# Kernel tuning notes

Measured on AMD Instinct MI355X. Metric: run time of the kernel, lower is better.

The kernel has to match this reference:

```python
import jax, jax.numpy as jnp
import numpy as np

EMBED = 1024
N_HEAD = 16
D_HID = EMBED // N_HEAD
R_FF = 4
D_FF = EMBED * R_FF
LN_EPS = 1e-5


def layer_norm(x, gamma, beta):
    mu = jnp.mean(x, axis=-1, keepdims=True)
    var = jnp.var(x, axis=-1, keepdims=True)
    return (x - mu) * jax.lax.rsqrt(var + LN_EPS) * gamma + beta


def setup_inputs() -> dict:
    key = jax.random.key(0)
    ks = jax.random.split(key, 10)
    B, S = 4, 2048
    # torch nn.Linear stores weight as [out, in]; y = x @ W.T
    def xavier(k, shape):
        fan_out, fan_in = shape
        lim = np.sqrt(6.0 / (fan_in + fan_out))
        return jax.random.uniform(k, shape, jnp.float32, -lim, lim)
    return {
        "x": jax.random.normal(ks[0], (B, S, EMBED), jnp.float32),
        "Wq": xavier(ks[1], (EMBED, EMBED)),
        "Wk": xavier(ks[2], (EMBED, EMBED)),
        "Wv": xavier(ks[3], (EMBED, EMBED)),
        "Wo": xavier(ks[4], (EMBED, EMBED)),
        "bo": jnp.zeros((EMBED,), jnp.float32),
        "ln1_g": jnp.ones((EMBED,), jnp.float32),
        "ln1_b": jnp.zeros((EMBED,), jnp.float32),
        "ln2_g": jnp.ones((EMBED,), jnp.float32),
        "ln2_b": jnp.zeros((EMBED,), jnp.float32),
        "W1": jax.random.normal(ks[5], (D_FF, EMBED), jnp.float32) * np.sqrt(2.0 / EMBED),
        "b1": jnp.zeros((D_FF,), jnp.float32),
        "W2": xavier(ks[6], (EMBED, D_FF)),
        "b2": jnp.zeros((EMBED,), jnp.float32),
    }


def reference(x, Wq, Wk, Wv, Wo, bo, ln1_g, ln1_b, ln2_g, ln2_b, W1, b1, W2, b2):
    B, S, E = x.shape
    scaling = 1.0 / np.sqrt(D_HID)
    # --- attention (pre-LN), dropout = identity (eval) ---
    xn = layer_norm(x, ln1_g, ln1_b)
    q = (xn @ Wq.T).reshape(B, S, N_HEAD, D_HID) * scaling
    k = (xn @ Wk.T).reshape(B, S, N_HEAD, D_HID)
    v = (xn @ Wv.T).reshape(B, S, N_HEAD, D_HID)
    scores = jnp.einsum("bqhd,bkhd->bhqk", q, k)
    attn = jax.nn.softmax(scores, axis=-1)
    out = jnp.einsum("bhqk,bkhd->bqhd", attn, v).reshape(B, S, E)
    out = out @ Wo.T + bo
    x = x + out
    # --- feed-forward (pre-LN) ---
    xn = layer_norm(x, ln2_g, ln2_b)
    h = jax.nn.relu(xn @ W1.T + b1)
    x = x + (h @ W2.T + b2)
    return x
```

## Files before the change

kernel.cpp:

```cpp
#include <hip/hip_runtime.h>
#include <hip/hip_bf16.h>
#include <cstdint>


typedef __attribute__((ext_vector_type(8))) short bf16x8;
typedef __attribute__((ext_vector_type(4))) float f32x4;

#define LDSAS __attribute__((address_space(3)))
#define GLBAS __attribute__((address_space(1)))

#define CQK 0.18033688011112044f

union APU { unsigned u[4]; bf16x8 v; };

__device__ __forceinline__ unsigned short f2bf(float f) {
  union { float f; unsigned u; } c; c.f = f;
  unsigned u = c.u + 0x7fffu + ((c.u >> 16) & 1u);
  return (unsigned short)(u >> 16);
}

__device__ __forceinline__ unsigned pk2(float a, float b) {
  __hip_bfloat162 h = __float22bfloat162_rn(make_float2(a, b));
  union { __hip_bfloat162 h; unsigned u; } c; c.h = h; return c.u;
}

__device__ __forceinline__ void async16(const unsigned short* g, unsigned short* l) {
  __builtin_amdgcn_global_load_lds((const GLBAS unsigned int*)g,
                                   (LDSAS unsigned int*)l, 16, 0, 0);
}

__global__ void cvt_all(const float* __restrict__ q, const float* __restrict__ k,
                        const float* __restrict__ v, const float* __restrict__ o,
                        const float* __restrict__ w1, const float* __restrict__ w2,
                        unsigned short* __restrict__ wsb) {
  const long i = (long)blockIdx.x * 256 + threadIdx.x;
  const float* src; unsigned short* dst; long off;
  if (i < 1048576) {
    const long seg = i >> 18, o4 = i & 262143;
    src = (seg == 0) ? q : (seg == 1) ? k : (seg == 2) ? v : o;
    dst = wsb + ((seg == 3) ? 3145728L : seg * 1048576L);
    off = o4;
  } else if (i < 2097152) {
    src = w1; dst = wsb + 4194304; off = i - 1048576;
  } else {
    src = w2; dst = wsb + 8388608; off = i - 2097152;
  }
  const float4 vv = ((const float4*)src)[off];
  ushort4 r;
  r.x = f2bf(vv.x); r.y = f2bf(vv.y); r.z = f2bf(vv.z); r.w = f2bf(vv.w);
  ((ushort4*)dst)[off] = r;
}

__global__ void ln_fwd(const float* __restrict__ x, const float* __restrict__ g,
                       const float* __restrict__ bb, unsigned short* __restrict__ outp) {
  const int row = blockIdx.x, tid = threadIdx.x;
  const float4 v = ((const float4*)(x + (long)row * 1024))[tid];
  float s  = v.x + v.y + v.z + v.w;
  float sq = v.x * v.x + v.y * v.y + v.z * v.z + v.w * v.w;
#pragma unroll
  for (int off = 1; off < 64; off <<= 1) {
    s  += __shfl_xor(s, off);
    sq += __shfl_xor(sq, off);
  }
  __shared__ float red[8];
  const int wv = tid >> 6, lane = tid & 63;
  if (lane == 0) { red[wv] = s; red[4 + wv] = sq; }
  __syncthreads();
  s  = red[0] + red[1] + red[2] + red[3];
  sq = red[4] + red[5] + red[6] + red[7];
  const float mu  = s * (1.f / 1024.f);
  const float var = sq * (1.f / 1024.f) - mu * mu;
  const float rstd = rsqrtf(var + 1e-5f);
  const float4 gv = ((const float4*)g)[tid];
  const float4 bv = ((const float4*)bb)[tid];
  ushort4 o;
  o.x = f2bf((v.x - mu) * rstd * gv.x + bv.x);
  o.y = f2bf((v.y - mu) * rstd * gv.y + bv.y);
  o.z = f2bf((v.z - mu) * rstd * gv.z + bv.z);
  o.w = f2bf((v.w - mu) * rstd * gv.w + bv.w);
  ((ushort4*)(outp + (long)row * 1024))[tid] = o;
}

template <int EPI>
__launch_bounds__(256, 3)
__global__ void gemm_bt(const unsigned short* __restrict__ A,
                        const unsigned short* __restrict__ B,
                        void* __restrict__ Cout,
                        const float* __restrict__ bias,
                        const float* __restrict__ res,
                        unsigned short* __restrict__ vt4,
                        int M, int N, int K) {
  __shared__ __align__(16) unsigned short As[128 * 64];
  __shared__ __align__(16) unsigned short Bs[128 * 64];
  const int tid  = threadIdx.x;
  const int lane = tid & 63;
  const int wvu  = __builtin_amdgcn_readfirstlane(tid >> 6);
  const int quad = lane >> 4, l16 = lane & 15;
  const int wm = wvu >> 1, wn = wvu & 1;

  const int gx = gridDim.x;
  const int id = blockIdx.y * gx + blockIdx.x;
  const int xcd = id & 7, slot = id >> 3;
  const int by = xcd * 8 + (slot & 7);
  const int bx = slot >> 3;
  const long m0 = (long)by * 128, n0 = (long)bx * 128;

  f32x4 acc[4][4];
#pragma unroll
  for (int i = 0; i < 4; i++)
#pragma unroll
    for (int j = 0; j < 4; j++) acc[i][j] = (f32x4){0.f, 0.f, 0.f, 0.f};

  const int rxA = l16 & 7;
  const int c0A = quad ^ rxA;
  int srow[4], sgc[4];
#pragma unroll
  for (int j = 0; j < 4; ++j) {
    const int s = wvu * 256 + j * 64 + lane;
    srow[j] = s >> 3;
    sgc[j] = ((s & 7) ^ (srow[j] & 7)) * 8;
  }

  for (int k0 = 0; k0 < K; k0 += 64) {
    __syncthreads();
#pragma unroll
    for (int j = 0; j < 4; ++j) {
      const int db = (wvu * 256 + j * 64) * 8;
      async16(A + (m0 + srow[j]) * K + k0 + sgc[j], As + db);
      async16(B + (n0 + srow[j]) * K + k0 + sgc[j], Bs + db);
    }
    __syncthreads();

#pragma unroll
    for (int kc = 0; kc < 2; ++kc) {
      const int ch = (c0A ^ (kc * 4)) * 8;
      bf16x8 af[4], bfr[4];
#pragma unroll
      for (int t = 0; t < 4; ++t) {
        af[t]  = *(const bf16x8*)(As + (wm * 64 + t * 16 + l16) * 64 + ch);
        bfr[t] = *(const bf16x8*)(Bs + (wn * 64 + t * 16 + l16) * 64 + ch);
      }
#pragma unroll
      for (int mt = 0; mt < 4; ++mt)
#pragma unroll
        for (int nt = 0; nt < 4; ++nt)
          acc[mt][nt] = __builtin_amdgcn_mfma_f32_16x16x32_bf16(af[mt], bfr[nt],
                                                                acc[mt][nt], 0, 0, 0);
    }
  }

  if (EPI == 3) {
#pragma unroll
    for (int nt = 0; nt < 4; ++nt) {
      const long col = n0 + wn * 64 + nt * 16 + l16;
      if (col < 2048) {
        const float scl = (col < 1024) ? CQK : 1.0f;
#pragma unroll
        for (int mt = 0; mt < 4; ++mt)
#pragma unroll
          for (int r = 0; r < 4; ++r) {
            const long row = m0 + wm * 64 + mt * 16 + quad * 4 + r;
            ((unsigned short*)Cout)[row * (long)N + col] = f2bf(acc[mt][nt][r] * scl);
          }
      } else {
        const int hd = (int)(col - 2048);
        const int h = hd >> 6, d = hd & 63;
        const int dsw = d + (d >> 2);
#pragma unroll
        for (int mt = 0; mt < 4; ++mt) {
          const long row = m0 + wm * 64 + mt * 16 + quad * 4;
          const int b_ = (int)(row >> 11);
          const int kv = (int)(row & 2047);
          const int t32 = kv >> 5;
          const int q_ = (kv >> 2) & 3;
          const int tt = (kv >> 4) & 1;
          const int c = d * 4 + ((q_ + dsw) & 3);
          ushort4 o;
          o.x = f2bf(acc[mt][nt][0]);
          o.y = f2bf(acc[mt][nt][1]);
          o.z = f2bf(acc[mt][nt][2]);
          o.w = f2bf(acc[mt][nt][3]);
          *(ushort4*)(vt4 + ((long)((b_ * 16 + h) * 64 + t32)) * 2048 + c * 8 + tt * 4) = o;
        }
      }
    }
  } else {
#pragma unroll
    for (int nt = 0; nt < 4; ++nt) {
      const long col = n0 + wn * 64 + nt * 16 + l16;
      float bv = 0.f;
      if (EPI == 1 || EPI == 2) bv = bias[col];
#pragma unroll
      for (int mt = 0; mt < 4; ++mt) {
#pragma unroll
        for (int r = 0; r < 4; ++r) {
          const long row = m0 + wm * 64 + mt * 16 + quad * 4 + r;
          const long idx = row * (long)N + col;
          float v = acc[mt][nt][r];
          if (EPI == 0) {
            ((unsigned short*)Cout)[idx] = f2bf(v);
          } else if (EPI == 1) {
            ((float*)Cout)[idx] = v + bv + res[idx];
          } else {
            v += bv;
            ((unsigned short*)Cout)[idx] = f2bf(v > 0.f ? v : 0.f);
          }
        }
      }
    }
  }
}

#define W2_LDA(AF, BUF, H)                                                      \
  do {                                                                          \
    const unsigned short* _p = As + ((BUF) * 2 + (H)) * 4096;                   \
    _Pragma("unroll") for (int _m = 0; _m < 2; ++_m) {                          \
      AF[_m][0] = *(const bf16x8*)(_p + (_m * 32 + rA) * 64 + chk0);            \
      AF[_m][1] = *(const bf16x8*)(_p + (_m * 32 + rA) * 64 + chk1);            \
    }                                                                           \
  } while (0)

#define W2_LDB(BF, BUF, H)                                                      \
  do {                                                                          \
    const unsigned short* _p = Bs + ((BUF) * 2 + (H)) * 8192;                   \
    _Pragma("unroll") for (int _n = 0; _n < 2; ++_n) {                          \
      BF[_n][0] = *(const bf16x8*)(_p + (_n * 64 + rB) * 64 + chk0);            \
      BF[_n][1] = *(const bf16x8*)(_p + (_n * 64 + rB) * 64 + chk1);            \
    }                                                                           \
  } while (0)

#define W2_MFMA(AH, BH, AF, BF)                                                 \
  do {                                                                          \
    _Pragma("unroll") for (int _m = 0; _m < 2; ++_m)                            \
    _Pragma("unroll") for (int _n = 0; _n < 2; ++_n) {                          \
      acc[(AH) * 2 + _m][(BH) * 2 + _n] =                                       \
          __builtin_amdgcn_mfma_f32_16x16x32_bf16(                              \
              AF[_m][0], BF[_n][0], acc[(AH) * 2 + _m][(BH) * 2 + _n], 0, 0, 0);\
      acc[(AH) * 2 + _m][(BH) * 2 + _n] =                                       \
          __builtin_amdgcn_mfma_f32_16x16x32_bf16(                              \
              AF[_m][1], BF[_n][1], acc[(AH) * 2 + _m][(BH) * 2 + _n], 0, 0, 0);\
    }                                                                           \
  } while (0)

#define PH_MID()                                                                \
  __builtin_amdgcn_s_barrier();                                                 \
  asm volatile("s_waitcnt lgkmcnt(0)" ::: "memory");                            \
  __builtin_amdgcn_sched_barrier(0);                                            \
  __builtin_amdgcn_s_setprio(1)

#define PH_END()                                                                \
  __builtin_amdgcn_s_setprio(0);                                                \
  __builtin_amdgcn_sched_barrier(0);                                            \
  __builtin_amdgcn_s_barrier();                                                 \
  __builtin_amdgcn_sched_barrier(0)

__launch_bounds__(512, 2)
__global__ void gemm_w2(const unsigned short* __restrict__ A,
                        const unsigned short* __restrict__ B,
                        float* __restrict__ Cout,
                        const float* __restrict__ bias,
                        const float* __restrict__ res,
                        int M, int N, int K) {
  extern __shared__ __align__(16) unsigned short lds[];
  unsigned short* As = lds;
  unsigned short* Bs = lds + 16384;

  const int tid  = threadIdx.x;
  const int lane = tid & 63;
  const int wv   = __builtin_amdgcn_readfirstlane(tid >> 6);
  const int quad = lane >> 4, l16 = lane & 15;
  const int wm = wv >> 2, wn = wv & 3;

  const int id = blockIdx.x;
  const int xcd = id & 7, slot = id >> 3;
  const int by = xcd * 8 + (slot & 7);
  const int bx = slot >> 3;
  const long m0 = (long)by * 128, n0 = (long)bx * 256;

  const int s0 = wv * 64 + lane;
  const int r0 = s0 >> 3;
  const int c0 = (s0 ^ r0) & 7;
  const int s1 = 512 + s0;
  const int r1 = s1 >> 3;
  const int c1 = (s1 ^ r1) & 7;
  const long rt0 = (long)r0 * K + c0 * 8;
  const long rt1 = (long)r1 * K + c1 * 8;
  const unsigned short* Ab = A + m0 * K;
  const unsigned short* Bb = B + n0 * K;

  const int rA = wm * 16 + l16;
  const int rB = wn * 16 + l16;
  const int chk0 = (quad ^ (l16 & 7)) * 8;
  const int chk1 = chk0 ^ 32;

  f32x4 acc[4][4];
#pragma unroll
  for (int a_ = 0; a_ < 4; ++a_)
#pragma unroll
    for (int b_ = 0; b_ < 4; ++b_) acc[a_][b_] = (f32x4){0.f, 0.f, 0.f, 0.f};

  auto stgA = [&](int b, int h, long kk) {
    const unsigned short* s = Ab + (long)h * 64 * K + kk;
    async16(s + rt0, As + (b * 2 + h) * 4096 + wv * 512);
  };
  auto stgB = [&](int b, int h, long kk) {
    const unsigned short* s = Bb + (long)h * 128 * K + kk;
    unsigned short* d = Bs + (b * 2 + h) * 8192 + wv * 512;
    async16(s + rt0, d);
    async16(s + rt1, d + 4096);
  };

  stgA(0, 0, 0); stgB(0, 1, 0); stgA(0, 1, 0); stgB(0, 0, 0);
  stgA(1, 0, 64); stgB(1, 1, 64); stgA(1, 1, 64);
  asm volatile("s_waitcnt vmcnt(4)" ::: "memory");
  __builtin_amdgcn_s_barrier();
  __builtin_amdgcn_sched_barrier(0);

  const int NI = K >> 7;
  for (int it = 0; it < NI; ++it) {
    const long kt  = (long)it * 128;
    const long ku  = kt + 64;
    const long kt2 = kt + 128;
    const long kt3 = kt + 192;
    const bool more = (it + 1 < NI);

    {
      bf16x8 a0[2][2], a1[2][2], b0[2][2], b1[2][2];
      W2_LDA(a0, 0, 0); W2_LDB(b0, 0, 0);
      stgB(1, 0, ku);
      PH_MID();
      W2_MFMA(0, 0, a0, b0);
      PH_END();
      W2_LDB(b1, 0, 1);
      if (more) stgA(0, 0, kt2);
      PH_MID();
      W2_MFMA(0, 1, a0, b1);
      PH_END();
      W2_LDA(a1, 0, 1);
      if (more) stgB(0, 1, kt2);
      PH_MID();
      W2_MFMA(1, 1, a1, b1);
      PH_END();
      W2_LDB(b0, 0, 0);
      if (more) stgA(0, 1, kt2);
      PH_MID();
      W2_MFMA(1, 0, a1, b0);
      __builtin_amdgcn_s_setprio(0);
      __builtin_amdgcn_sched_barrier(0);
      if (more) { asm volatile("s_waitcnt vmcnt(4)" ::: "memory"); }
      else      { asm volatile("s_waitcnt vmcnt(0)" ::: "memory"); }
      __builtin_amdgcn_s_barrier();
      __builtin_amdgcn_sched_barrier(0);
    }
    {
      bf16x8 a0[2][2], a1[2][2], b0[2][2], b1[2][2];
      W2_LDA(a0, 1, 0); W2_LDB(b0, 1, 0);
      if (more) stgB(0, 0, kt2);
      PH_MID();
      W2_MFMA(0, 0, a0, b0);
      PH_END();
      W2_LDB(b1, 1, 1);
      if (more) stgA(1, 0, kt3);
      PH_MID();
      W2_MFMA(0, 1, a0, b1);
      PH_END();
      W2_LDA(a1, 1, 1);
      if (more) stgB(1, 1, kt3);
      PH_MID();
      W2_MFMA(1, 1, a1, b1);
      PH_END();
      W2_LDB(b0, 1, 0);
      if (more) stgA(1, 1, kt3);
      PH_MID();
      W2_MFMA(1, 0, a1, b0);
      __builtin_amdgcn_s_setprio(0);
      __builtin_amdgcn_sched_barrier(0);
      if (more) { asm volatile("s_waitcnt vmcnt(4)" ::: "memory"); }
      __builtin_amdgcn_s_barrier();
      __builtin_amdgcn_sched_barrier(0);
    }
  }

#pragma unroll
  for (int nt = 0; nt < 4; ++nt) {
    const long col = n0 + nt * 64 + wn * 16 + l16;
    const float bv = bias[col];
#pragma unroll
    for (int mt = 0; mt < 4; ++mt) {
#pragma unroll
      for (int r = 0; r < 4; ++r) {
        const long row = m0 + mt * 32 + wm * 16 + quad * 4 + r;
        const long idx = row * (long)N + col;
        Cout[idx] = acc[mt][nt][r] + bv + res[idx];
      }
    }
  }
}

__launch_bounds__(256, 8)
__global__ void attn_fwd(const unsigned short* __restrict__ qkv,
                         const unsigned short* __restrict__ vt,
                         unsigned short* __restrict__ outp) {
  __shared__ __align__(16) unsigned short lds[10240];

  const int tid = threadIdx.x;
  const int lane = tid & 63;
  const int wv = __builtin_amdgcn_readfirstlane(tid >> 6);
  const int quad = lane >> 4, l16 = lane & 15;

  const int id = blockIdx.y * 32 + blockIdx.x;
  const int xcd = id & 7, slot = id >> 3;
  const int bh = xcd * 8 + (slot >> 5);
  const int qt = slot & 31;
  const int b = bh >> 4, h = bh & 15;
  const long rowbase = (long)b * 2048;
  const int hoff = h * 64;

  const int rot0 = (quad + l16) & 7;
  const int rot1 = rot0 ^ 4;

  bf16x8 bq0, bq1;
  {
    const long qrow = rowbase + qt * 64 + wv * 16 + l16;
    const unsigned short* qp = qkv + qrow * 3072 + hoff;
    bq0 = *(const bf16x8*)(qp + quad * 8);
    bq1 = *(const bf16x8*)(qp + (quad ^ 4) * 8);
  }
  __builtin_amdgcn_sched_barrier(0);

  const int c0 = wv * 64 + lane;
  const int r0 = c0 >> 3;
  const int ks = ((c0 & 7) - r0) & 7;
  const unsigned short* kptr = qkv + (rowbase + r0) * 3072 + 1024 + hoff + ks * 8;
  const unsigned short* vptr = vt + (long)bh * 131072 + (long)c0 * 8;

  auto stage = [&](int t) {
    unsigned short* kdst = lds + ((t & 1) << 11) + wv * 512;
    unsigned short* vdst = lds + 4096 + ((t % 3) << 11) + wv * 512;
    async16(kptr + (long)t * 32 * 3072, kdst);
    async16(vptr + (long)t * 2048, vdst);
  };

  bf16x8 ones;
#pragma unroll
  for (int i = 0; i < 8; ++i) ones[i] = (short)0x3F80;

  f32x4 oacc[4], lacc;
  lacc = (f32x4){0.f, 0.f, 0.f, 0.f};
#pragma unroll
  for (int i = 0; i < 4; ++i) oacc[i] = (f32x4){0.f, 0.f, 0.f, 0.f};

  auto QK = [&](int t, f32x4 (&sx)[2]) {
    const unsigned short* Kb = lds + ((t & 1) << 11);
    __builtin_amdgcn_s_setprio(1);
#pragma unroll
    for (int tt = 0; tt < 2; ++tt) {
      const int ar = tt * 16 + l16;
      bf16x8 ak0 = *(const bf16x8*)(Kb + ar * 64 + rot0 * 8);
      bf16x8 ak1 = *(const bf16x8*)(Kb + ar * 64 + rot1 * 8);
      f32x4 z = (f32x4){0.f, 0.f, 0.f, 0.f};
      z = __builtin_amdgcn_mfma_f32_16x16x32_bf16(ak0, bq0, z, 0, 0, 0);
      sx[tt] = __builtin_amdgcn_mfma_f32_16x16x32_bf16(ak1, bq1, z, 0, 0, 0);
    }
    __builtin_amdgcn_s_setprio(0);
  };

  auto SM = [&](f32x4 (&sx)[2], APU& ap) {
#pragma unroll
    for (int tt = 0; tt < 2; ++tt) {
      const f32x4 sv = sx[tt];
      const float p0 = __builtin_amdgcn_exp2f(sv[0]);
      const float p1 = __builtin_amdgcn_exp2f(sv[1]);
      const float p2 = __builtin_amdgcn_exp2f(sv[2]);
      const float p3 = __builtin_amdgcn_exp2f(sv[3]);
      ap.u[tt * 2 + 0] = pk2(p0, p1);
      ap.u[tt * 2 + 1] = pk2(p2, p3);
    }
    lacc = __builtin_amdgcn_mfma_f32_16x16x32_bf16(ap.v, ones, lacc, 0, 0, 0);
  };

  auto PV = [&](int t, APU& ap) {
    const unsigned short* Vb = lds + 4096 + ((t % 3) << 11);
    __builtin_amdgcn_s_setprio(1);
#pragma unroll
    for (int dt = 0; dt < 4; ++dt) {
      const int d = dt * 16 + l16;
      const int rotv = (quad + d + (d >> 2)) & 3;
      bf16x8 bv = *(const bf16x8*)(Vb + d * 32 + rotv * 8);
      oacc[dt] = __builtin_amdgcn_mfma_f32_16x16x32_bf16(ap.v, bv, oacc[dt], 0, 0, 0);
    }
    __builtin_amdgcn_s_setprio(0);
  };

  auto body = [&](int kt, f32x4 (&scur)[2], f32x4 (&snxt)[2], bool qknext) {
    const bool more = (kt + 2 < 64);
    if (more) stage(kt + 2);
    APU ap;
    SM(scur, ap);
    if (more) { asm volatile("s_waitcnt vmcnt(2)" ::: "memory"); }
    else      { asm volatile("s_waitcnt vmcnt(0)" ::: "memory"); }
    __builtin_amdgcn_s_barrier();
    __builtin_amdgcn_sched_barrier(0);
    PV(kt, ap);
    if (qknext) QK(kt + 1, snxt);
    __builtin_amdgcn_s_barrier();
    __builtin_amdgcn_sched_barrier(0);
  };

  stage(0); stage(1);
  asm volatile("s_waitcnt vmcnt(2)" ::: "memory");
  __builtin_amdgcn_s_barrier();
  __builtin_amdgcn_sched_barrier(0);

  f32x4 sacc0[2], sacc1[2];
  QK(0, sacc0);
  __builtin_amdgcn_s_barrier();
  __builtin_amdgcn_sched_barrier(0);

  for (int it = 0; it < 32; ++it) {
    body(2 * it,     sacc0, sacc1, true);
    body(2 * it + 1, sacc1, sacc0, it < 31);
  }

  float linv[4];
#pragma unroll
  for (int r = 0; r < 4; ++r) linv[r] = 1.f / lacc[r];
#pragma unroll
  for (int dt = 0; dt < 4; ++dt)
#pragma unroll
    for (int r = 0; r < 4; ++r) {
      const long row = rowbase + qt * 64 + wv * 16 + quad * 4 + r;
      outp[row * 1024 + hoff + dt * 16 + l16] = f2bf(oacc[dt][r] * linv[r]);
    }
}

extern "C" void kernel_launch(void* const* d_in, const int* in_sizes, int n_in,
                              void* d_out, int out_size, void* d_ws, size_t ws_size,
                              hipStream_t stream) {
  (void)in_sizes; (void)n_in; (void)out_size; (void)ws_size;
  const float* x   = (const float*)d_in[0];
  const float* Wq  = (const float*)d_in[1];
  const float* Wk  = (const float*)d_in[2];
  const float* Wv  = (const float*)d_in[3];
  const float* Wo  = (const float*)d_in[4];
  const float* bo  = (const float*)d_in[5];
  const float* g1  = (const float*)d_in[6];
  const float* be1 = (const float*)d_in[7];
  const float* g2  = (const float*)d_in[8];
  const float* be2 = (const float*)d_in[9];
  const float* W1  = (const float*)d_in[10];
  const float* bf1 = (const float*)d_in[11];
  const float* W2  = (const float*)d_in[12];
  const float* bf2 = (const float*)d_in[13];

  static bool s_attr = false;
  if (!s_attr) {
    hipFuncSetAttribute(reinterpret_cast<const void*>(&gemm_w2),
                        hipFuncAttributeMaxDynamicSharedMemorySize, 98304);
    s_attr = true;
  }

  char* ws = (char*)d_ws;
  unsigned short* wqkv  = (unsigned short*)(ws);
  unsigned short* wo    = (unsigned short*)(ws + 6291456);
  unsigned short* w1    = (unsigned short*)(ws + 8388608);
  unsigned short* w2    = (unsigned short*)(ws + 16777216);
  unsigned short* xn    = (unsigned short*)(ws + 25165824);
  unsigned short* big   = (unsigned short*)(ws + 41943040);
  unsigned short* vtg   = (unsigned short*)(ws + 92274688);
  unsigned short* attnb = (unsigned short*)(ws + 109051904);
  float*          x1    = (float*)(ws + 125829120);

  cvt_all<<<12288, 256, 0, stream>>>(Wq, Wk, Wv, Wo, W1, W2, wqkv);

  ln_fwd<<<8192, 256, 0, stream>>>(x, g1, be1, xn);
  gemm_bt<3><<<dim3(24, 64), 256, 0, stream>>>(xn, wqkv, big, nullptr, nullptr,
                                               vtg, 8192, 3072, 1024);
  attn_fwd<<<dim3(32, 64), 256, 0, stream>>>(big, vtg, attnb);
  gemm_bt<1><<<dim3(8, 64), 256, 0, stream>>>(attnb, wo, x1, bo, x,
                                              nullptr, 8192, 1024, 1024);
  ln_fwd<<<8192, 256, 0, stream>>>(x1, g2, be2, xn);
  gemm_bt<2><<<dim3(32, 64), 256, 0, stream>>>(xn, w1, big, bf1, nullptr,
                                               nullptr, 8192, 4096, 1024);
  gemm_w2<<<dim3(256), 512, 98304, stream>>>(big, w2, (float*)d_out, bf2, x1,
                                             8192, 1024, 4096);
}
```

Baseline: 453.2 us.

## Double attention tile sizes: 128 queries per block, 64-key KV tiles

The attention kernel now uses 8 waves (512 threads) per block covering 128 query rows, and processes 64 keys per pipeline step instead of 32, halving the number of barrier-separated iterations. The transposed-V layout written by the QKV GEMM epilogue is reworked to match the 64-key tiles with a new swizzle, and LDS doubles to 40 KB. The aim is to amortize K/V staging and synchronization over more queries and keys, at the cost of fewer blocks, more registers per wave and possible occupancy loss.

```diff
diff --git a/kernel.cpp b/kernel.cpp
--- a/kernel.cpp
+++ b/kernel.cpp
@@ -165,22 +165,23 @@
       } else {
         const int hd = (int)(col - 2048);
         const int h = hd >> 6, d = hd & 63;
-        const int dsw = d + (d >> 2);
 #pragma unroll
         for (int mt = 0; mt < 4; ++mt) {
           const long row = m0 + wm * 64 + mt * 16 + quad * 4;
           const int b_ = (int)(row >> 11);
           const int kv = (int)(row & 2047);
-          const int t32 = kv >> 5;
-          const int q_ = (kv >> 2) & 3;
-          const int tt = (kv >> 4) & 1;
-          const int c = d * 4 + ((q_ + dsw) & 3);
+          const int t_ = kv >> 6;
+          const int sk = kv & 63;
+          const int kvp4 = (sk & 32) | ((sk & 16) >> 2) | ((sk & 8) << 1) | ((sk & 4) << 1);
+          const int kk = kvp4 >> 3, half = (kvp4 >> 2) & 1;
+          const int cc = d * 8 + ((kk + d) & 7);
+          const int u = cc * 2 + half;
           ushort4 o;
           o.x = f2bf(acc[mt][nt][0]);
           o.y = f2bf(acc[mt][nt][1]);
           o.z = f2bf(acc[mt][nt][2]);
           o.w = f2bf(acc[mt][nt][3]);
-          *(ushort4*)(vt4 + ((long)((b_ * 16 + h) * 64 + t32)) * 2048 + c * 8 + tt * 4) = o;
+          *(ushort4*)(vt4 + ((long)((b_ * 16 + h) * 32 + t_)) * 4096 + u * 4) = o;
         }
       }
     }
@@ -397,21 +398,21 @@
   }
 }
 
-__launch_bounds__(256, 8)
+__launch_bounds__(512, 8)
 __global__ void attn_fwd(const unsigned short* __restrict__ qkv,
                          const unsigned short* __restrict__ vt,
                          unsigned short* __restrict__ outp) {
-  __shared__ __align__(16) unsigned short lds[10240];
+  __shared__ __align__(16) unsigned short lds[20480];
 
   const int tid = threadIdx.x;
   const int lane = tid & 63;
   const int wv = __builtin_amdgcn_readfirstlane(tid >> 6);
   const int quad = lane >> 4, l16 = lane & 15;
 
-  const int id = blockIdx.y * 32 + blockIdx.x;
+  const int id = blockIdx.y * 16 + blockIdx.x;
   const int xcd = id & 7, slot = id >> 3;
-  const int bh = xcd * 8 + (slot >> 5);
-  const int qt = slot & 31;
+  const int bh = xcd * 8 + (slot >> 4);
+  const int qt = slot & 15;
   const int b = bh >> 4, h = bh & 15;
   const long rowbase = (long)b * 2048;
   const int hoff = h * 64;
@@ -421,7 +422,7 @@
 
   bf16x8 bq0, bq1;
   {
-    const long qrow = rowbase + qt * 64 + wv * 16 + l16;
+    const long qrow = rowbase + qt * 128 + wv * 16 + l16;
     const unsigned short* qp = qkv + qrow * 3072 + hoff;
     bq0 = *(const bf16x8*)(qp + quad * 8);
     bq1 = *(const bf16x8*)(qp + (quad ^ 4) * 8);
@@ -435,10 +436,10 @@
   const unsigned short* vptr = vt + (long)bh * 131072 + (long)c0 * 8;
 
   auto stage = [&](int t) {
-    unsigned short* kdst = lds + ((t & 1) << 11) + wv * 512;
-    unsigned short* vdst = lds + 4096 + ((t % 3) << 11) + wv * 512;
-    async16(kptr + (long)t * 32 * 3072, kdst);
-    async16(vptr + (long)t * 2048, vdst);
+    unsigned short* kdst = lds + (t & 1) * 4096 + wv * 512;
+    unsigned short* vdst = lds + 8192 + (t % 3) * 4096 + wv * 512;
+    async16(kptr + (long)t * 64 * 3072, kdst);
+    async16(vptr + (long)t * 4096, vdst);
   };
 
   bf16x8 ones;
@@ -450,11 +451,11 @@
 #pragma unroll
   for (int i = 0; i < 4; ++i) oacc[i] = (f32x4){0.f, 0.f, 0.f, 0.f};
 
-  auto QK = [&](int t, f32x4 (&sx)[2]) {
-    const unsigned short* Kb = lds + ((t & 1) << 11);
+  auto QK = [&](int t, f32x4 (&sx)[4]) {
+    const unsigned short* Kb = lds + (t & 1) * 4096;
     __builtin_amdgcn_s_setprio(1);
 #pragma unroll
-    for (int tt = 0; tt < 2; ++tt) {
+    for (int tt = 0; tt < 4; ++tt) {
       const int ar = tt * 16 + l16;
       bf16x8 ak0 = *(const bf16x8*)(Kb + ar * 64 + rot0 * 8);
       bf16x8 ak1 = *(const bf16x8*)(Kb + ar * 64 + rot1 * 8);
@@ -465,37 +466,43 @@
     __builtin_amdgcn_s_setprio(0);
   };
 
-  auto SM = [&](f32x4 (&sx)[2], APU& ap) {
-#pragma unroll
-    for (int tt = 0; tt < 2; ++tt) {
-      const f32x4 sv = sx[tt];
-      const float p0 = __builtin_amdgcn_exp2f(sv[0]);
-      const float p1 = __builtin_amdgcn_exp2f(sv[1]);
-      const float p2 = __builtin_amdgcn_exp2f(sv[2]);
-      const float p3 = __builtin_amdgcn_exp2f(sv[3]);
-      ap.u[tt * 2 + 0] = pk2(p0, p1);
-      ap.u[tt * 2 + 1] = pk2(p2, p3);
-    }
-    lacc = __builtin_amdgcn_mfma_f32_16x16x32_bf16(ap.v, ones, lacc, 0, 0, 0);
-  };
-
-  auto PV = [&](int t, APU& ap) {
-    const unsigned short* Vb = lds + 4096 + ((t % 3) << 11);
+  auto SM = [&](f32x4 (&sx)[4], APU (&ap)[2]) {
+#pragma unroll
+    for (int hf = 0; hf < 2; ++hf) {
+#pragma unroll
+      for (int tt = 0; tt < 2; ++tt) {
+        const f32x4 sv = sx[hf * 2 + tt];
+        const float p0 = __builtin_amdgcn_exp2f(sv[0]);
+        const float p1 = __builtin_amdgcn_exp2f(sv[1]);
+        const float p2 = __builtin_amdgcn_exp2f(sv[2]);
+        const float p3 = __builtin_amdgcn_exp2f(sv[3]);
+        ap[hf].u[tt * 2 + 0] = pk2(p0, p1);
+        ap[hf].u[tt * 2 + 1] = pk2(p2, p3);
+      }
+      lacc = __builtin_amdgcn_mfma_f32_16x16x32_bf16(ap[hf].v, ones, lacc, 0, 0, 0);
+    }
+  };
+
+  auto PV = [&](int t, APU (&ap)[2]) {
+    const unsigned short* Vb = lds + 8192 + (t % 3) * 4096;
     __builtin_amdgcn_s_setprio(1);
 #pragma unroll
-    for (int dt = 0; dt < 4; ++dt) {
-      const int d = dt * 16 + l16;
-      const int rotv = (quad + d + (d >> 2)) & 3;
-      bf16x8 bv = *(const bf16x8*)(Vb + d * 32 + rotv * 8);
-      oacc[dt] = __builtin_amdgcn_mfma_f32_16x16x32_bf16(ap.v, bv, oacc[dt], 0, 0, 0);
+    for (int hf = 0; hf < 2; ++hf) {
+      const int vbase = (hf ? rot1 : rot0) * 8;
+#pragma unroll
+      for (int dt = 0; dt < 4; ++dt) {
+        bf16x8 bv = *(const bf16x8*)(Vb + vbase + (dt * 16 + l16) * 64);
+        oacc[dt] = __builtin_amdgcn_mfma_f32_16x16x32_bf16(ap[hf].v, bv,
+                                                           oacc[dt], 0, 0, 0);
+      }
     }
     __builtin_amdgcn_s_setprio(0);
   };
 
-  auto body = [&](int kt, f32x4 (&scur)[2], f32x4 (&snxt)[2], bool qknext) {
-    const bool more = (kt + 2 < 64);
+  auto body = [&](int kt, f32x4 (&scur)[4], f32x4 (&snxt)[4], bool qknext) {
+    const bool more = (kt + 2 < 32);
     if (more) stage(kt + 2);
-    APU ap;
+    APU ap[2];
     SM(scur, ap);
     if (more) { asm volatile("s_waitcnt vmcnt(2)" ::: "memory"); }
     else      { asm volatile("s_waitcnt vmcnt(0)" ::: "memory"); }
@@ -512,14 +519,14 @@
   __builtin_amdgcn_s_barrier();
   __builtin_amdgcn_sched_barrier(0);
 
-  f32x4 sacc0[2], sacc1[2];
+  f32x4 sacc0[4], sacc1[4];
   QK(0, sacc0);
   __builtin_amdgcn_s_barrier();
   __builtin_amdgcn_sched_barrier(0);
 
-  for (int it = 0; it < 32; ++it) {
+  for (int it = 0; it < 16; ++it) {
     body(2 * it,     sacc0, sacc1, true);
-    body(2 * it + 1, sacc1, sacc0, it < 31);
+    body(2 * it + 1, sacc1, sacc0, it < 15);
   }
 
   float linv[4];
@@ -529,7 +536,7 @@
   for (int dt = 0; dt < 4; ++dt)
 #pragma unroll
     for (int r = 0; r < 4; ++r) {
-      const long row = rowbase + qt * 64 + wv * 16 + quad * 4 + r;
+      const long row = rowbase + qt * 128 + wv * 16 + quad * 4 + r;
       outp[row * 1024 + hoff + dt * 16 + l16] = f2bf(oacc[dt][r] * linv[r]);
     }
 }
@@ -576,7 +583,7 @@
   ln_fwd<<<8192, 256, 0, stream>>>(x, g1, be1, xn);
   gemm_bt<3><<<dim3(24, 64), 256, 0, stream>>>(xn, wqkv, big, nullptr, nullptr,
                                                vtg, 8192, 3072, 1024);
-  attn_fwd<<<dim3(32, 64), 256, 0, stream>>>(big, vtg, attnb);
+  attn_fwd<<<dim3(16, 64), 512, 0, stream>>>(big, vtg, attnb);
   gemm_bt<1><<<dim3(8, 64), 256, 0, stream>>>(attnb, wo, x1, bo, x,
                                               nullptr, 8192, 1024, 1024);
   ln_fwd<<<8192, 256, 0, stream>>>(x1, g2, be2, xn);
```

Measured after the change: 469.5 us. 3.6% more time.
